# Kernel optimization log

Measured on AMD Instinct MI355X. Metric: run time of the kernel, lower is better.

## Reference

```python
import jax, jax.numpy as jnp
import numpy as np

B, C, H, W = 8, 512, 64, 64


def setup_inputs() -> dict:
    key = jax.random.key(0)
    ks = jax.random.split(key, 8)
    return {
        "query": jax.random.normal(ks[0], (B, C, H, W), jnp.float32),
        "key": jax.random.normal(ks[1], (B, C, H, W), jnp.float32),
        "value": jax.random.normal(ks[2], (B, C, H, W), jnp.float32),
        "w1": jax.random.normal(ks[3], (4 * C, C), jnp.float32) * 0.02,
        "b1": jax.random.normal(ks[4], (4 * C,), jnp.float32) * 0.02,
        "w2": jax.random.normal(ks[5], (C, 4 * C), jnp.float32) * 0.02,
        "b2": jax.random.normal(ks[6], (C,), jnp.float32) * 0.02,
        "gamma": jax.random.normal(ks[7], (1,), jnp.float32),
    }


def reference(query, key, value, w1, b1, w2, b2, gamma):
    b, c, h, w = query.shape
    scale = c ** (-0.5)
    # flatten spatial dims: tokens n = h*w, channels c
    q = query.reshape(b, c, -1)   # [B,C,N]
    k = key.reshape(b, c, -1)     # [B,C,N]
    v = value.reshape(b, c, -1)   # [B,C,N]
    # attn[b,n,m] = softmax_m(q_n . k_m * scale)
    attn = jax.nn.softmax(jnp.einsum('bcn,bcm->bnm', q, k) * scale, axis=-1)
    out = jnp.einsum('bnm,bcm->bcn', attn, v).reshape(b, c, h, w)
    # 1x1-conv FFN: C -> 4C -> C with ReLU
    hdn = jax.nn.relu(jnp.einsum('bchw,dc->bdhw', out, w1) + b1[None, :, None, None])
    ffn = jnp.einsum('bdhw,cd->bchw', hdn, w2) + b2[None, :, None, None]
    return ffn * gamma + query
```

## Files before the change

### kernel.cpp

```cpp
#include <hip/hip_runtime.h>
#include <hip/hip_bf16.h>
#include <stdint.h>

#define BB 8
#define CC 512
#define NN 4096
#define QB 64
#define KB 64
#define D4 2048
#define NT (NN / KB)

typedef short bf8 __attribute__((ext_vector_type(8)));
typedef float f32x4 __attribute__((ext_vector_type(4)));

__device__ __forceinline__ uint16_t f2bf(float f) {
  uint32_t u = __builtin_bit_cast(uint32_t, f);
  u = (u + 0x7FFFu + ((u >> 16) & 1u)) >> 16;
  return (uint16_t)u;
}
__device__ __forceinline__ float bf2f(uint16_t u) {
  return __builtin_bit_cast(float, (uint32_t)u << 16);
}

__device__ __forceinline__ void gl_lds16(const void* g, void* l) {
  __builtin_amdgcn_global_load_lds((__attribute__((address_space(1))) void*)g,
                                   (__attribute__((address_space(3))) void*)l, 16, 0, 0);
}

__global__ __launch_bounds__(256) void transpose_cast_k(const float* __restrict__ src,
                                                        uint16_t* __restrict__ dst,
                                                        float scale) {
  __shared__ float tile[32][33];
  int b = blockIdx.z;
  int n0 = blockIdx.x * 32, c0 = blockIdx.y * 32;
  int tx = threadIdx.x & 31, ty = threadIdx.x >> 5;
  const float* s = src + ((size_t)b * CC + c0) * NN + n0;
#pragma unroll
  for (int i = 0; i < 4; i++) {
    int c = ty + i * 8;
    tile[tx][c] = s[(size_t)c * NN + tx];
  }
  __syncthreads();
  uint16_t* d = dst + ((size_t)b * NN + n0) * CC + c0;
#pragma unroll
  for (int i = 0; i < 4; i++) {
    int n = ty + i * 8;
    d[(size_t)n * CC + tx] = f2bf(tile[n][tx] * scale);
  }
}

__global__ __launch_bounds__(256) void cast_k(const float* __restrict__ in,
                                              uint16_t* __restrict__ out, int n) {
  int i = (blockIdx.x * 256 + threadIdx.x) * 4;
  if (i >= n) return;
  float4 v = *(const float4*)(in + i);
  ushort4 o;
  o.x = f2bf(v.x); o.y = f2bf(v.y); o.z = f2bf(v.z); o.w = f2bf(v.w);
  *(ushort4*)(out + i) = o;
}

__global__ __launch_bounds__(256) void vpack_k(const float* __restrict__ v,
                                               uint16_t* __restrict__ vp) {
  const int blk = blockIdx.x;
  const int w = blk & 7, mtb = blk >> 3;
  const int mt = mtb & (NT - 1), b = mtb >> 6;
  const int tid = threadIdx.x;
#pragma unroll
  for (int h = 0; h < 2; h++) {
    const int c = tid + h * 256;
    const int ks = c >> 8, rt = (c >> 6) & 3, l = c & 63;
    const int llo = l & 15, lhi = l >> 4;
    const float* src = v + ((size_t)b * CC + w * 64 + rt * 16 + llo) * NN + mt * 64 + ks * 32 + lhi * 8;
    const float4 f0 = *(const float4*)src;
    const float4 f1 = *(const float4*)(src + 4);
    ushort4 o0, o1;
    o0.x = f2bf(f0.x); o0.y = f2bf(f0.y); o0.z = f2bf(f0.z); o0.w = f2bf(f0.w);
    o1.x = f2bf(f1.x); o1.y = f2bf(f1.y); o1.z = f2bf(f1.z); o1.w = f2bf(f1.w);
    uint16_t* dst = vp + (size_t)blk * 4096 + ks * 2048 + rt * 512 + l * 8;
    *(ushort4*)dst = o0;
    *(ushort4*)(dst + 4) = o1;
  }
}

__global__ __launch_bounds__(512) __attribute__((amdgpu_waves_per_eu(2, 2))) void attn_ffn_k(
    const uint16_t* __restrict__ Qt, const uint16_t* __restrict__ Kt,
    const uint16_t* __restrict__ Vp, const uint16_t* __restrict__ W1b,
    const uint16_t* __restrict__ W2b, const float* __restrict__ b1,
    const float* __restrict__ b2, const float* __restrict__ gma,
    const float* __restrict__ qry, float* __restrict__ out) {
  __shared__ __attribute__((aligned(16))) uint16_t Ks[2][KB][CC];
  __shared__ __attribute__((aligned(16))) uint16_t SP[QB][72];
  __shared__ __attribute__((aligned(16))) uint16_t Ps[QB][KB];
  __shared__ float lst[QB];
  __shared__ float rsc[QB];

  const int bid = blockIdx.x + gridDim.x * blockIdx.y;
  const int b = bid & 7;
  const int n0 = (bid >> 3) * QB;
  const int tid = threadIdx.x;
  const int lane = tid & 63, wid = tid >> 6;
  const int lhi = lane >> 4, llo = lane & 15;
  const int r7 = llo & 7;

  const int srt = wid >> 1;
  const int sct0 = (wid & 1) * 2;

  bf8 qf[16];
  {
    const uint16_t* qsrc = Qt + ((size_t)b * NN + n0 + srt * 16 + llo) * CC + lhi * 8;
#pragma unroll
    for (int kc = 0; kc < 16; kc++) qf[kc] = *(const bf8*)(qsrc + kc * 32);
  }

#pragma unroll
  for (int j = 0; j < 8; j++) {
    const int r = wid * 8 + j;
    gl_lds16(Kt + ((size_t)b * NN + r) * CC + ((lane ^ (r & 7)) << 3), &Ks[0][r][0]);
  }

  const f32x4 vzero = {0.f, 0.f, 0.f, 0.f};
  f32x4 acc[4][4];
#pragma unroll
  for (int i = 0; i < 4; i++)
#pragma unroll
    for (int j = 0; j < 4; j++) acc[i][j] = vzero;

  const uint16_t* vpw = Vp + (size_t)b * ((size_t)NT * 8 * 4096) + wid * 4096 + lane * 8;
  const int srow = tid >> 3, sj = tid & 7;
  float m_run = -__builtin_inff(), l_run = 0.f;
  bf8 av[2][4];

  auto QK = [&](int cur, int dummy) {
    const uint16_t* k0row = &Ks[cur][sct0 * 16 + llo][0];
    const uint16_t* k1row = &Ks[cur][sct0 * 16 + 16 + llo][0];
    f32x4 s0 = vzero, s1 = vzero;
#pragma unroll
    for (int kc = 0; kc < 16; kc++) {
      const int g = ((kc * 4 + lhi) ^ r7) << 3;
      bf8 bk0 = *(const bf8*)(k0row + g);
      bf8 bk1 = *(const bf8*)(k1row + g);
      s0 = __builtin_amdgcn_mfma_f32_16x16x32_bf16(qf[kc], bk0, s0, 0, 0, 0);
      s1 = __builtin_amdgcn_mfma_f32_16x16x32_bf16(qf[kc], bk1, s1, 0, 0, 0);
    }
    const int n = srt * 16 + lhi * 4;
#pragma unroll
    for (int r = 0; r < 4; r++) {
      SP[n + r][sct0 * 16 + llo] = f2bf(s0[r]);
      SP[n + r][sct0 * 16 + 16 + llo] = f2bf(s1[r]);
    }
  };

  auto SOFTMAX = [&](bool last) {
    const bf8 sv8 = *(const bf8*)&SP[srow][sj * 8];
    float sv[8];
#pragma unroll
    for (int k2 = 0; k2 < 8; k2++) sv[k2] = bf2f((uint16_t)sv8[k2]);
    float mx = fmaxf(fmaxf(fmaxf(sv[0], sv[1]), fmaxf(sv[2], sv[3])),
                     fmaxf(fmaxf(sv[4], sv[5]), fmaxf(sv[6], sv[7])));
    mx = fmaxf(mx, __shfl_xor(mx, 1, 8));
    mx = fmaxf(mx, __shfl_xor(mx, 2, 8));
    mx = fmaxf(mx, __shfl_xor(mx, 4, 8));
    const float nm = fmaxf(m_run, mx);
    const float rs = __expf(m_run - nm);
    float p[8], psum = 0.f;
#pragma unroll
    for (int k2 = 0; k2 < 8; k2++) {
      p[k2] = __expf(sv[k2] - nm);
      psum += p[k2];
    }
    bf8 pk;
#pragma unroll
    for (int k2 = 0; k2 < 8; k2++) pk[k2] = (short)f2bf(p[k2]);
    *(bf8*)(&Ps[srow][0] + ((sj ^ (srow & 7)) << 3)) = pk;
    psum += __shfl_xor(psum, 1, 8);
    psum += __shfl_xor(psum, 2, 8);
    psum += __shfl_xor(psum, 4, 8);
    l_run = l_run * rs + psum;
    m_run = nm;
    if (sj == 0) {
      rsc[srow] = rs;
      if (last) lst[srow] = l_run;
    }
  };

  auto PV = [&](int dummy) {
    float rsn[4];
#pragma unroll
    for (int nt = 0; nt < 4; nt++) rsn[nt] = rsc[nt * 16 + llo];
#pragma unroll
    for (int rt = 0; rt < 4; rt++)
#pragma unroll
      for (int nt = 0; nt < 4; nt++) acc[rt][nt] *= rsn[nt];
#pragma unroll
    for (int ks = 0; ks < 2; ks++) {
      bf8 bp[4];
#pragma unroll
      for (int nt = 0; nt < 4; nt++)
        bp[nt] = *(const bf8*)(&Ps[nt * 16 + llo][0] + ((((ks << 2) + lhi) ^ r7) << 3));
#pragma unroll
      for (int rt = 0; rt < 4; rt++)
#pragma unroll
        for (int nt = 0; nt < 4; nt++)
          acc[rt][nt] = __builtin_amdgcn_mfma_f32_16x16x32_bf16(av[ks][rt], bp[nt], acc[rt][nt], 0, 0, 0);
    }
  };

  auto VLOAD = [&](int t) {
    const uint16_t* vt = vpw + (size_t)t * 32768;
#pragma unroll
    for (int ks = 0; ks < 2; ks++)
#pragma unroll
      for (int rt = 0; rt < 4; rt++)
        av[ks][rt] = *(const bf8*)(vt + ks * 2048 + rt * 512);
  };

  auto KDMA = [&](int t, int buf) {
#pragma unroll
    for (int j = 0; j < 8; j++) {
      const int r = wid * 8 + j;
      gl_lds16(Kt + ((size_t)b * NN + t * KB + r) * CC + ((lane ^ (r & 7)) << 3),
               &Ks[buf][r][0]);
    }
  };

  asm volatile("s_waitcnt vmcnt(0)" ::: "memory");
  __builtin_amdgcn_s_barrier();
  __builtin_amdgcn_s_setprio(1);
  QK(0, 0);
  __builtin_amdgcn_s_setprio(0);
  VLOAD(0);
  KDMA(1, 1);
  asm volatile("s_waitcnt lgkmcnt(0)" ::: "memory");
  __builtin_amdgcn_s_barrier();

  for (int t = 1; t < NT; t++) {
    const int cur = t & 1;
    SOFTMAX(false);
    asm volatile("s_waitcnt vmcnt(0)" ::: "memory");
    __builtin_amdgcn_s_barrier();
    __builtin_amdgcn_s_setprio(1);
    PV(0);
    QK(cur, 0);
    __builtin_amdgcn_s_setprio(0);
    VLOAD(t);
    if (t + 1 < NT) KDMA(t + 1, cur ^ 1);
    asm volatile("s_waitcnt lgkmcnt(0)" ::: "memory");
    __builtin_amdgcn_s_barrier();
  }

  SOFTMAX(true);
  asm volatile("s_waitcnt vmcnt(0)" ::: "memory");
  __builtin_amdgcn_s_barrier();
  __builtin_amdgcn_s_setprio(1);
  PV(0);
  __builtin_amdgcn_s_setprio(0);

  __syncthreads();

  float invl[4];
#pragma unroll
  for (int nt = 0; nt < 4; nt++) invl[nt] = 1.0f / lst[nt * 16 + llo];

  uint16_t(*Old)[CC] = (uint16_t(*)[CC]) & Ks[0][0][0];
#pragma unroll
  for (int rt = 0; rt < 4; rt++)
#pragma unroll
    for (int nt = 0; nt < 4; nt++) {
      ushort4 o4;
      o4.x = f2bf(acc[rt][nt][0] * invl[nt]);
      o4.y = f2bf(acc[rt][nt][1] * invl[nt]);
      o4.z = f2bf(acc[rt][nt][2] * invl[nt]);
      o4.w = f2bf(acc[rt][nt][3] * invl[nt]);
      const int gch = wid * 8 + rt * 2 + (lhi >> 1);
      *(ushort4*)(&Old[nt * 16 + llo][0] + ((gch ^ r7) << 3) + ((lhi & 1) << 2)) = o4;
    }

  uint16_t(*Hs)[CC] = (uint16_t(*)[CC]) & Ks[1][0][0];
  f32x4 facc[4][4];
#pragma unroll
  for (int i = 0; i < 4; i++)
#pragma unroll
    for (int j = 0; j < 4; j++) facc[i][j] = vzero;
  const float g = gma[0];
  const uint16_t* orow[4];
  const uint16_t* hrow[4];
#pragma unroll
  for (int nt = 0; nt < 4; nt++) {
    orow[nt] = &Old[nt * 16 + llo][0];
    hrow[nt] = &Hs[nt * 16 + llo][0];
  }

  for (int qtr = 0; qtr < 4; qtr++) {
    const int dq0 = qtr * 512;
    f32x4 hacc[4][4];
#pragma unroll
    for (int i = 0; i < 4; i++)
#pragma unroll
      for (int j = 0; j < 4; j++) hacc[i][j] = vzero;
    __syncthreads();
    __builtin_amdgcn_s_setprio(1);
#pragma unroll 2
    for (int kc8 = 0; kc8 < 64; kc8 += 4) {
      bf8 bo[4], aw[4];
      const int gof = ((kc8 + lhi) ^ r7) << 3;
#pragma unroll
      for (int nt = 0; nt < 4; nt++) bo[nt] = *(const bf8*)(orow[nt] + gof);
#pragma unroll
      for (int dt = 0; dt < 4; dt++) {
        const int d = dq0 + wid * 64 + dt * 16 + llo;
        aw[dt] = *(const bf8*)(W1b + (size_t)d * CC + (kc8 + lhi) * 8);
      }
#pragma unroll
      for (int dt = 0; dt < 4; dt++)
#pragma unroll
        for (int nt = 0; nt < 4; nt++)
          hacc[dt][nt] = __builtin_amdgcn_mfma_f32_16x16x32_bf16(aw[dt], bo[nt], hacc[dt][nt], 0, 0, 0);
    }
    __builtin_amdgcn_s_setprio(0);
#pragma unroll
    for (int dt = 0; dt < 4; dt++) {
      const int dg = dq0 + wid * 64 + dt * 16 + lhi * 4;
      const float4 b1v = *(const float4*)(b1 + dg);
#pragma unroll
      for (int nt = 0; nt < 4; nt++) {
        ushort4 h4;
        h4.x = f2bf(fmaxf(hacc[dt][nt][0] + b1v.x, 0.f));
        h4.y = f2bf(fmaxf(hacc[dt][nt][1] + b1v.y, 0.f));
        h4.z = f2bf(fmaxf(hacc[dt][nt][2] + b1v.z, 0.f));
        h4.w = f2bf(fmaxf(hacc[dt][nt][3] + b1v.w, 0.f));
        const int gch = wid * 8 + dt * 2 + (lhi >> 1);
        *(ushort4*)(&Hs[nt * 16 + llo][0] + ((gch ^ r7) << 3) + ((lhi & 1) << 2)) = h4;
      }
    }
    __syncthreads();
    __builtin_amdgcn_s_setprio(1);
#pragma unroll 2
    for (int kd8 = 0; kd8 < 64; kd8 += 4) {
      bf8 ah[4], bw[4];
      const int gof = ((kd8 + lhi) ^ r7) << 3;
#pragma unroll
      for (int nt = 0; nt < 4; nt++) ah[nt] = *(const bf8*)(hrow[nt] + gof);
#pragma unroll
      for (int ct = 0; ct < 4; ct++) {
        const int c = wid * 64 + ct * 16 + llo;
        bw[ct] = *(const bf8*)(W2b + (size_t)c * D4 + dq0 + (kd8 + lhi) * 8);
      }
#pragma unroll
      for (int nt = 0; nt < 4; nt++)
#pragma unroll
        for (int ct = 0; ct < 4; ct++)
          facc[nt][ct] = __builtin_amdgcn_mfma_f32_16x16x32_bf16(ah[nt], bw[ct], facc[nt][ct], 0, 0, 0);
    }
    __builtin_amdgcn_s_setprio(0);
  }

#pragma unroll
  for (int nt = 0; nt < 4; nt++) {
    const int n = n0 + nt * 16 + lhi * 4;
#pragma unroll
    for (int ct = 0; ct < 4; ct++) {
      const int c = wid * 64 + ct * 16 + llo;
      const float b2c = b2[c];
      const size_t off = ((size_t)b * CC + c) * NN + n;
      const float4 q4 = *(const float4*)(qry + off);
      float4 o4;
      o4.x = (facc[nt][ct][0] + b2c) * g + q4.x;
      o4.y = (facc[nt][ct][1] + b2c) * g + q4.y;
      o4.z = (facc[nt][ct][2] + b2c) * g + q4.z;
      o4.w = (facc[nt][ct][3] + b2c) * g + q4.w;
      *(float4*)(out + off) = o4;
    }
  }
}

extern "C" void kernel_launch(void* const* d_in, const int* in_sizes, int n_in,
                              void* d_out, int out_size, void* d_ws, size_t ws_size,
                              hipStream_t stream) {
  const float* q = (const float*)d_in[0];
  const float* k = (const float*)d_in[1];
  const float* v = (const float*)d_in[2];
  const float* w1 = (const float*)d_in[3];
  const float* b1 = (const float*)d_in[4];
  const float* w2 = (const float*)d_in[5];
  const float* b2 = (const float*)d_in[6];
  const float* gm = (const float*)d_in[7];
  float* out = (float*)d_out;

  uint16_t* Qt = (uint16_t*)d_ws;
  uint16_t* Kt = Qt + (size_t)BB * NN * CC;
  uint16_t* Vp = Kt + (size_t)BB * NN * CC;
  uint16_t* W1b = Vp + (size_t)BB * NN * CC;
  uint16_t* W2b = W1b + (size_t)D4 * CC;

  dim3 tgrid(NN / 32, CC / 32, BB);
  transpose_cast_k<<<tgrid, 256, 0, stream>>>(q, Qt, 0.044194173824159216f);
  transpose_cast_k<<<tgrid, 256, 0, stream>>>(k, Kt, 1.0f);
  vpack_k<<<BB * NT * 8, 256, 0, stream>>>(v, Vp);
  cast_k<<<(D4 * CC / 4 + 255) / 256, 256, 0, stream>>>(w1, W1b, D4 * CC);
  cast_k<<<(CC * D4 / 4 + 255) / 256, 256, 0, stream>>>(w2, W2b, CC * D4);
  attn_ffn_k<<<dim3(NN / QB, BB), 512, 0, stream>>>(Qt, Kt, Vp, W1b, W2b, b1, b2, gm, q, out);
}
```

Before: 724.0 us.

## Pipeline attention stages three-deep with rotating score/probability buffers

Replaces the two-stage QK/softmax/PV schedule with a three-stage software pipeline. Each iteration computes QK for tile t, softmax for tile t-1 and PV for tile t-2, using three rotating SP/rsc buffers, with probabilities written in place over the scores. This removes one barrier per tile and lets softmax overlap the matrix work of other waves. The V loads move to the start of the iteration, so they now wait within the same iteration instead of across one. The P layout drops its XOR swizzle, which may add LDS bank conflicts.

```diff
diff --git a/kernel.cpp b/kernel.cpp
--- a/kernel.cpp
+++ b/kernel.cpp
@@ -85,14 +85,13 @@
 __global__ __launch_bounds__(512) __attribute__((amdgpu_waves_per_eu(2, 2))) void attn_ffn_k(
     const uint16_t* __restrict__ Qt, const uint16_t* __restrict__ Kt,
     const uint16_t* __restrict__ Vp, const uint16_t* __restrict__ W1b,
-    const uint16_t* __restrict__ W2b, const float* __restrict__ b1,
+    const uint16_t* __restrict__ W2b, const float* __restrict__ b1v_,
     const float* __restrict__ b2, const float* __restrict__ gma,
     const float* __restrict__ qry, float* __restrict__ out) {
   __shared__ __attribute__((aligned(16))) uint16_t Ks[2][KB][CC];
-  __shared__ __attribute__((aligned(16))) uint16_t SP[QB][72];
-  __shared__ __attribute__((aligned(16))) uint16_t Ps[QB][KB];
+  __shared__ __attribute__((aligned(16))) uint16_t SP[3][QB][72];
+  __shared__ float rsc[3][QB];
   __shared__ float lst[QB];
-  __shared__ float rsc[QB];
 
   const int bid = blockIdx.x + gridDim.x * blockIdx.y;
   const int b = bid & 7;
@@ -130,9 +129,9 @@
   float m_run = -__builtin_inff(), l_run = 0.f;
   bf8 av[2][4];
 
-  auto QK = [&](int cur, int dummy) {
-    const uint16_t* k0row = &Ks[cur][sct0 * 16 + llo][0];
-    const uint16_t* k1row = &Ks[cur][sct0 * 16 + 16 + llo][0];
+  auto QK = [&](int kbuf, int sb) {
+    const uint16_t* k0row = &Ks[kbuf][sct0 * 16 + llo][0];
+    const uint16_t* k1row = &Ks[kbuf][sct0 * 16 + 16 + llo][0];
     f32x4 s0 = vzero, s1 = vzero;
 #pragma unroll
     for (int kc = 0; kc < 16; kc++) {
@@ -145,13 +144,13 @@
     const int n = srt * 16 + lhi * 4;
 #pragma unroll
     for (int r = 0; r < 4; r++) {
-      SP[n + r][sct0 * 16 + llo] = f2bf(s0[r]);
-      SP[n + r][sct0 * 16 + 16 + llo] = f2bf(s1[r]);
+      SP[sb][n + r][sct0 * 16 + llo] = f2bf(s0[r]);
+      SP[sb][n + r][sct0 * 16 + 16 + llo] = f2bf(s1[r]);
     }
   };
 
-  auto SOFTMAX = [&](bool last) {
-    const bf8 sv8 = *(const bf8*)&SP[srow][sj * 8];
+  auto SOFTMAX = [&](int sb, bool last) {
+    const bf8 sv8 = *(const bf8*)&SP[sb][srow][sj * 8];
     float sv[8];
 #pragma unroll
     for (int k2 = 0; k2 < 8; k2++) sv[k2] = bf2f((uint16_t)sv8[k2]);
@@ -171,22 +170,22 @@
     bf8 pk;
 #pragma unroll
     for (int k2 = 0; k2 < 8; k2++) pk[k2] = (short)f2bf(p[k2]);
-    *(bf8*)(&Ps[srow][0] + ((sj ^ (srow & 7)) << 3)) = pk;
+    *(bf8*)&SP[sb][srow][sj * 8] = pk;
     psum += __shfl_xor(psum, 1, 8);
     psum += __shfl_xor(psum, 2, 8);
     psum += __shfl_xor(psum, 4, 8);
     l_run = l_run * rs + psum;
     m_run = nm;
     if (sj == 0) {
-      rsc[srow] = rs;
+      rsc[sb][srow] = rs;
       if (last) lst[srow] = l_run;
     }
   };
 
-  auto PV = [&](int dummy) {
+  auto PV = [&](int sb) {
     float rsn[4];
 #pragma unroll
-    for (int nt = 0; nt < 4; nt++) rsn[nt] = rsc[nt * 16 + llo];
+    for (int nt = 0; nt < 4; nt++) rsn[nt] = rsc[sb][nt * 16 + llo];
 #pragma unroll
     for (int rt = 0; rt < 4; rt++)
 #pragma unroll
@@ -196,7 +195,7 @@
       bf8 bp[4];
 #pragma unroll
       for (int nt = 0; nt < 4; nt++)
-        bp[nt] = *(const bf8*)(&Ps[nt * 16 + llo][0] + ((((ks << 2) + lhi) ^ r7) << 3));
+        bp[nt] = *(const bf8*)&SP[sb][nt * 16 + llo][(ks * 4 + lhi) * 8];
 #pragma unroll
       for (int rt = 0; rt < 4; rt++)
 #pragma unroll
@@ -225,34 +224,48 @@
 
   asm volatile("s_waitcnt vmcnt(0)" ::: "memory");
   __builtin_amdgcn_s_barrier();
+
+  KDMA(1, 1);
   __builtin_amdgcn_s_setprio(1);
   QK(0, 0);
   __builtin_amdgcn_s_setprio(0);
-  VLOAD(0);
-  KDMA(1, 1);
-  asm volatile("s_waitcnt lgkmcnt(0)" ::: "memory");
+  asm volatile("s_waitcnt vmcnt(0) lgkmcnt(0)" ::: "memory");
   __builtin_amdgcn_s_barrier();
 
-  for (int t = 1; t < NT; t++) {
-    const int cur = t & 1;
-    SOFTMAX(false);
-    asm volatile("s_waitcnt vmcnt(0)" ::: "memory");
+  KDMA(2, 0);
+  SOFTMAX(0, false);
+  __builtin_amdgcn_s_setprio(1);
+  QK(1, 1);
+  __builtin_amdgcn_s_setprio(0);
+  asm volatile("s_waitcnt vmcnt(0) lgkmcnt(0)" ::: "memory");
+  __builtin_amdgcn_s_barrier();
+
+  int sb0 = 2, sb1 = 1, sb2 = 0;
+  for (int t = 2; t < NT; t++) {
+    VLOAD(t - 2);
+    if (t + 1 < NT) KDMA(t + 1, (t + 1) & 1);
+    SOFTMAX(sb1, false);
+    __builtin_amdgcn_s_setprio(1);
+    PV(sb2);
+    QK(t & 1, sb0);
+    __builtin_amdgcn_s_setprio(0);
+    asm volatile("s_waitcnt vmcnt(0) lgkmcnt(0)" ::: "memory");
     __builtin_amdgcn_s_barrier();
-    __builtin_amdgcn_s_setprio(1);
-    PV(0);
-    QK(cur, 0);
-    __builtin_amdgcn_s_setprio(0);
-    VLOAD(t);
-    if (t + 1 < NT) KDMA(t + 1, cur ^ 1);
-    asm volatile("s_waitcnt lgkmcnt(0)" ::: "memory");
-    __builtin_amdgcn_s_barrier();
-  }
-
-  SOFTMAX(true);
-  asm volatile("s_waitcnt vmcnt(0)" ::: "memory");
+    const int tb = sb2; sb2 = sb1; sb1 = sb0; sb0 = tb;
+  }
+
+  VLOAD(NT - 2);
+  SOFTMAX(sb1, true);
+  __builtin_amdgcn_s_setprio(1);
+  PV(sb2);
+  __builtin_amdgcn_s_setprio(0);
+  asm volatile("s_waitcnt vmcnt(0) lgkmcnt(0)" ::: "memory");
   __builtin_amdgcn_s_barrier();
+  { const int tb = sb2; sb2 = sb1; sb1 = sb0; sb0 = tb; }
+
+  VLOAD(NT - 1);
   __builtin_amdgcn_s_setprio(1);
-  PV(0);
+  PV(sb2);
   __builtin_amdgcn_s_setprio(0);
 
   __syncthreads();
@@ -320,7 +333,7 @@
 #pragma unroll
     for (int dt = 0; dt < 4; dt++) {
       const int dg = dq0 + wid * 64 + dt * 16 + lhi * 4;
-      const float4 b1v = *(const float4*)(b1 + dg);
+      const float4 b1v = *(const float4*)(b1v_ + dg);
 #pragma unroll
       for (int nt = 0; nt < 4; nt++) {
         ushort4 h4;
```

New measurement: 708.0 us. -2.2%, faster.
